# Kernel tuning notes

Measured on AMD Instinct MI355X. Metric: run time of the kernel, lower is better.

The kernel has to match this reference:

```python
import jax, jax.numpy as jnp
import numpy as np

# Module config (matches init_kwargs)
G, K, S = 64, 3, 2          # base patch size, num scales, scale factor
B, H, W, C = 64, 512, 512, 3
HG, HL = 128, 128
D_IN = K * G * G * C


def setup_inputs() -> dict:
    key = jax.random.key(0)
    kx, kl, k1, k2 = jax.random.split(key, 4)
    x = jax.random.normal(kx, (B, H, W, C), dtype=jnp.float32)
    # glimpse locations in [-1, 1)
    l = jax.random.uniform(kl, (B, 2), minval=-1.0, maxval=1.0, dtype=jnp.float32)
    # fc1: phi (D_IN -> HG); fc2: l (2 -> HL). PyTorch-Linear-like scale.
    W1 = jax.random.normal(k1, (D_IN, HG), dtype=jnp.float32) / np.sqrt(D_IN)
    b1 = jnp.zeros((HG,), dtype=jnp.float32)
    W2 = jax.random.normal(k2, (2, HL), dtype=jnp.float32) / np.sqrt(2.0)
    b2 = jnp.zeros((HL,), dtype=jnp.float32)
    return {"x": x, "l": l, "W1": W1, "b1": b1, "W2": W2, "b2": b2}


def _extract_glimpse(x, l):
    """Retina: k multi-scale patches centered at l, resized to (G,G).
    Returns (B, K, G, G, C)."""
    sizes = [G * S**i for i in range(K)]              # 64, 128, 256
    pad = sizes[-1] // 2 + 1                          # pad once for largest scale
    xp = jnp.pad(x, ((0, 0), (pad, pad), (pad, pad), (0, 0)))
    # denormalize: [-1,1] -> [0,H], truncated to int (torch .long())
    coords = (0.5 * (l + 1.0) * H).astype(jnp.int32)  # (B,2): col0=x, col1=y
    patches = []
    for size in sizes:
        fy = coords[:, 1] - size // 2 + pad
        fx = coords[:, 0] - size // 2 + pad

        def slice_one(img, y0, x0, size=size):
            return jax.lax.dynamic_slice(img, (y0, x0, 0), (size, size, C))

        p = jax.vmap(slice_one)(xp, fy, fx)           # (B, size, size, C)
        f = size // G
        if f > 1:  # downsample by integer factor via average pooling
            p = p.reshape(B, G, f, G, f, C).mean(axis=(2, 4))
        patches.append(p)
    return jnp.stack(patches, axis=1)                 # (B, K, G, G, C)


def reference(x, l, W1, b1, W2, b2):
    phi = _extract_glimpse(x, l).reshape(x.shape[0], -1)   # (B, K*G*G*C)
    phi_out = jax.nn.relu(phi @ W1 + b1)                   # (B, HG)
    l_out = jax.nn.relu(l @ W2 + b2)                       # (B, HL)
    return jax.nn.relu(jnp.concatenate([phi_out, l_out], axis=1))
```

## Files before the change

kernel.cpp:

```cpp
#include <hip/hip_runtime.h>
#include <hip/hip_bf16.h>

#define G_     64
#define NK     3
#define NB     64
#define IH     512
#define IW     512
#define NC     3
#define HG_    128
#define HL_    128
#define D_IN_    (NK * G_ * G_ * NC)
#define D_SCALE  (G_ * G_ * NC)
#define KCH      128
#define NCHUNK   (D_IN_ / KCH)
#define BSPLIT   4
#define NBLK     (NCHUNK * BSPLIT)
#define PSTRIDE  (NB * HG_)

template <int F>
__device__ __forceinline__ void scale_body(
    const float* __restrict__ x, const float* __restrict__ l,
    const float* __restrict__ W1, float* __restrict__ P,
    int roff, int d0, int b0, int chunkGlobal,
    float (&phi_s)[16][KCH], int* cx_s, int* cy_s)
{
    const int tid = threadIdx.x;
    if (tid < 16) {
        float lx = l[(b0 + tid) * 2 + 0];
        float ly = l[(b0 + tid) * 2 + 1];
        cx_s[tid] = (int)((0.5f * (lx + 1.0f)) * 512.0f);
        cy_s[tid] = (int)((0.5f * (ly + 1.0f)) * 512.0f);
    }
    __syncthreads();

    const int dd   = tid & (KCH - 1);
    const int jb0  = (tid >> 7) * 8;
    const int r    = roff + dd;
    const int gy   = r / (G_ * NC);
    const int rem  = r - gy * (G_ * NC);
    const int gx   = rem / NC;
    const int c    = rem - gx * NC;
    constexpr float inv = 1.0f / (float)(F * F);
    constexpr int JU = (F == 4) ? 2 : 8;

#pragma unroll 1
    for (int jo = 0; jo < 8; jo += JU) {
        float sums[JU];
#pragma unroll
        for (int ji = 0; ji < JU; ++ji) {
            const int jb = jb0 + jo + ji;
            const int b  = b0 + jb;
            const int by = cy_s[jb] - 32 * F + gy * F;
            const int bx = cx_s[jb] - 32 * F + gx * F;
            const float* bimg = x + (size_t)b * (IH * IW * NC) + c;
            float s = 0.0f;
#pragma unroll
            for (int dy = 0; dy < F; ++dy) {
                const int y = by + dy;
                const bool yok = (unsigned)y < (unsigned)IH;
#pragma unroll
                for (int dx = 0; dx < F; ++dx) {
                    const int xx = bx + dx;
                    const bool ok = yok && ((unsigned)xx < (unsigned)IW);
                    s += ok ? bimg[(size_t)y * (IW * NC) + xx * NC] : 0.0f;
                }
            }
            sums[ji] = s;
        }
#pragma unroll
        for (int ji = 0; ji < JU; ++ji)
            phi_s[jb0 + jo + ji][dd] = sums[ji] * inv;
    }
    __syncthreads();

    const int h0 = (tid & 31) * 4;
    const int bl = (tid >> 5) * 2;
    float a0[4] = {0, 0, 0, 0}, a1[4] = {0, 0, 0, 0};
    const float* wp = W1 + (size_t)d0 * HG_ + h0;
    const float4* prow0 = (const float4*)phi_s[bl];
    const float4* prow1 = (const float4*)phi_s[bl + 1];

#pragma unroll 2
    for (int t = 0; t < KCH / 4; ++t) {
        float4 p0v = prow0[t];
        float4 p1v = prow1[t];
#pragma unroll
        for (int u = 0; u < 4; ++u) {
            float4 wv = *(const float4*)(wp + (size_t)(4 * t + u) * HG_);
            float p0 = (&p0v.x)[u];
            float p1 = (&p1v.x)[u];
            a0[0] = fmaf(p0, wv.x, a0[0]);
            a0[1] = fmaf(p0, wv.y, a0[1]);
            a0[2] = fmaf(p0, wv.z, a0[2]);
            a0[3] = fmaf(p0, wv.w, a0[3]);
            a1[0] = fmaf(p1, wv.x, a1[0]);
            a1[1] = fmaf(p1, wv.y, a1[1]);
            a1[2] = fmaf(p1, wv.z, a1[2]);
            a1[3] = fmaf(p1, wv.w, a1[3]);
        }
    }
    float* pb = P + (size_t)chunkGlobal * PSTRIDE + (b0 + bl) * HG_ + h0;
    *(float4*)pb            = make_float4(a0[0], a0[1], a0[2], a0[3]);
    *(float4*)(pb + HG_)    = make_float4(a1[0], a1[1], a1[2], a1[3]);
}

__global__ __launch_bounds__(256) void fused(
    const float* __restrict__ x, const float* __restrict__ l,
    const float* __restrict__ W1, float* __restrict__ P)
{
    __shared__ float phi_s[16][KCH];
    __shared__ int cx_s[16], cy_s[16];

    const int chunkGlobal = blockIdx.x >> 2;
    const int b0 = (blockIdx.x & 3) * 16;
    const int d0 = chunkGlobal * KCH;
    const int chunkLocal = chunkGlobal % 96;
    const int roff = chunkLocal * KCH;

    if (chunkGlobal < 96) {
        scale_body<1>(x, l, W1, P, roff, d0, b0, chunkGlobal, phi_s, cx_s, cy_s);
    } else if (chunkGlobal < 192) {
        scale_body<2>(x, l, W1, P, roff, d0, b0, chunkGlobal, phi_s, cx_s, cy_s);
    } else {
        scale_body<4>(x, l, W1, P, roff, d0, b0, chunkGlobal, phi_s, cx_s, cy_s);
    }
}

__global__ __launch_bounds__(256) void reduce_epilogue(
    const float* __restrict__ P,
    const float* __restrict__ l,
    const float* __restrict__ b1,
    const float* __restrict__ W2,
    const float* __restrict__ b2,
    float* __restrict__ out)
{
    __shared__ float red[HG_];
    const int b = blockIdx.x;
    const int t = threadIdx.x;
    const int h = t & (HG_ - 1);
    const int half = t >> 7;

    float s = 0.0f;
    const float* p = P + (size_t)(half * 144) * PSTRIDE + b * HG_ + h;
#pragma unroll 8
    for (int c = 0; c < 144; ++c)
        s += p[(size_t)c * PSTRIDE];

    if (half == 1) red[h] = s;
    __syncthreads();

    if (half == 0) {
        out[b * (HG_ + HL_) + h] = fmaxf(s + red[h] + b1[h], 0.0f);
    } else {
        float l0 = l[b * 2 + 0];
        float l1 = l[b * 2 + 1];
        float v = fmaf(l1, W2[HL_ + h], fmaf(l0, W2[h], b2[h]));
        out[b * (HG_ + HL_) + HG_ + h] = fmaxf(v, 0.0f);
    }
}

extern "C" void kernel_launch(void* const* d_in, const int* in_sizes, int n_in,
                              void* d_out, int out_size, void* d_ws, size_t ws_size,
                              hipStream_t stream) {
    const float* x  = (const float*)d_in[0];
    const float* l  = (const float*)d_in[1];
    const float* W1 = (const float*)d_in[2];
    const float* b1 = (const float*)d_in[3];
    const float* W2 = (const float*)d_in[4];
    const float* b2 = (const float*)d_in[5];
    float* out = (float*)d_out;
    float* P = (float*)d_ws;

    fused<<<NBLK, 256, 0, stream>>>(x, l, W1, P);
    reduce_epilogue<<<NB, 256, 0, stream>>>(P, l, b1, W2, b2, out);
}
```

Before: 288.5 us.

## Split K across thread groups in GEMM tile and widen reduce kernel with float4

The per-block GEMM now gives each thread 4 batch rows instead of 2 and splits the 128-wide K chunk between two halves of the block. The two halves' partials are combined through shared memory before the store. Each W1 load is therefore reused across more rows, at the cost of an extra sync and more shared memory. The reduce epilogue moves to 512 threads, with 16 groups reading float4 partials over 18 chunks each and a final shared-memory reduction, to raise memory-level parallelism.

```diff
diff --git a/kernel.cpp b/kernel.cpp
--- a/kernel.cpp
+++ b/kernel.cpp
@@ -1,5 +1,4 @@
 #include <hip/hip_runtime.h>
-#include <hip/hip_bf16.h>
 
 #define G_     64
 #define NK     3
@@ -22,7 +21,7 @@
     const float* __restrict__ x, const float* __restrict__ l,
     const float* __restrict__ W1, float* __restrict__ P,
     int roff, int d0, int b0, int chunkGlobal,
-    float (&phi_s)[16][KCH], int* cx_s, int* cy_s)
+    float (&phi_s)[16][KCH], float (&red2)[16][HG_], int* cx_s, int* cy_s)
 {
     const int tid = threadIdx.x;
     if (tid < 16) {
@@ -73,35 +72,65 @@
     }
     __syncthreads();
 
-    const int h0 = (tid & 31) * 4;
-    const int bl = (tid >> 5) * 2;
-    float a0[4] = {0, 0, 0, 0}, a1[4] = {0, 0, 0, 0};
-    const float* wp = W1 + (size_t)d0 * HG_ + h0;
-    const float4* prow0 = (const float4*)phi_s[bl];
-    const float4* prow1 = (const float4*)phi_s[bl + 1];
+    const int hq  = tid & 31;
+    const int h0  = hq * 4;
+    const int gg  = tid >> 5;
+    const int bg4 = (gg & 3) * 4;
+    const int dh  = gg >> 2;
+    const int db  = dh * 64;
+
+    float4 a0 = {0.f, 0.f, 0.f, 0.f};
+    float4 a1 = {0.f, 0.f, 0.f, 0.f};
+    float4 a2 = {0.f, 0.f, 0.f, 0.f};
+    float4 a3 = {0.f, 0.f, 0.f, 0.f};
+    const float* wp = W1 + (size_t)(d0 + db) * HG_ + h0;
 
 #pragma unroll 2
-    for (int t = 0; t < KCH / 4; ++t) {
-        float4 p0v = prow0[t];
-        float4 p1v = prow1[t];
+    for (int t = 0; t < 16; ++t) {
+        const float4 pv0 = *(const float4*)&phi_s[bg4 + 0][db + 4 * t];
+        const float4 pv1 = *(const float4*)&phi_s[bg4 + 1][db + 4 * t];
+        const float4 pv2 = *(const float4*)&phi_s[bg4 + 2][db + 4 * t];
+        const float4 pv3 = *(const float4*)&phi_s[bg4 + 3][db + 4 * t];
 #pragma unroll
         for (int u = 0; u < 4; ++u) {
-            float4 wv = *(const float4*)(wp + (size_t)(4 * t + u) * HG_);
-            float p0 = (&p0v.x)[u];
-            float p1 = (&p1v.x)[u];
-            a0[0] = fmaf(p0, wv.x, a0[0]);
-            a0[1] = fmaf(p0, wv.y, a0[1]);
-            a0[2] = fmaf(p0, wv.z, a0[2]);
-            a0[3] = fmaf(p0, wv.w, a0[3]);
-            a1[0] = fmaf(p1, wv.x, a1[0]);
-            a1[1] = fmaf(p1, wv.y, a1[1]);
-            a1[2] = fmaf(p1, wv.z, a1[2]);
-            a1[3] = fmaf(p1, wv.w, a1[3]);
+            const float4 wv = *(const float4*)(wp + (size_t)(4 * t + u) * HG_);
+            const float p0 = (&pv0.x)[u];
+            const float p1 = (&pv1.x)[u];
+            const float p2 = (&pv2.x)[u];
+            const float p3 = (&pv3.x)[u];
+            a0.x = fmaf(p0, wv.x, a0.x); a0.y = fmaf(p0, wv.y, a0.y);
+            a0.z = fmaf(p0, wv.z, a0.z); a0.w = fmaf(p0, wv.w, a0.w);
+            a1.x = fmaf(p1, wv.x, a1.x); a1.y = fmaf(p1, wv.y, a1.y);
+            a1.z = fmaf(p1, wv.z, a1.z); a1.w = fmaf(p1, wv.w, a1.w);
+            a2.x = fmaf(p2, wv.x, a2.x); a2.y = fmaf(p2, wv.y, a2.y);
+            a2.z = fmaf(p2, wv.z, a2.z); a2.w = fmaf(p2, wv.w, a2.w);
+            a3.x = fmaf(p3, wv.x, a3.x); a3.y = fmaf(p3, wv.y, a3.y);
+            a3.z = fmaf(p3, wv.z, a3.z); a3.w = fmaf(p3, wv.w, a3.w);
         }
     }
-    float* pb = P + (size_t)chunkGlobal * PSTRIDE + (b0 + bl) * HG_ + h0;
-    *(float4*)pb            = make_float4(a0[0], a0[1], a0[2], a0[3]);
-    *(float4*)(pb + HG_)    = make_float4(a1[0], a1[1], a1[2], a1[3]);
+
+    if (dh == 1) {
+        *(float4*)&red2[bg4 + 0][h0] = a0;
+        *(float4*)&red2[bg4 + 1][h0] = a1;
+        *(float4*)&red2[bg4 + 2][h0] = a2;
+        *(float4*)&red2[bg4 + 3][h0] = a3;
+    }
+    __syncthreads();
+    if (dh == 0) {
+        float* pb = P + (size_t)chunkGlobal * PSTRIDE + (size_t)(b0 + bg4) * HG_ + h0;
+        const float4 r0 = *(const float4*)&red2[bg4 + 0][h0];
+        const float4 r1 = *(const float4*)&red2[bg4 + 1][h0];
+        const float4 r2 = *(const float4*)&red2[bg4 + 2][h0];
+        const float4 r3 = *(const float4*)&red2[bg4 + 3][h0];
+        *(float4*)(pb + 0 * HG_) =
+            make_float4(a0.x + r0.x, a0.y + r0.y, a0.z + r0.z, a0.w + r0.w);
+        *(float4*)(pb + 1 * HG_) =
+            make_float4(a1.x + r1.x, a1.y + r1.y, a1.z + r1.z, a1.w + r1.w);
+        *(float4*)(pb + 2 * HG_) =
+            make_float4(a2.x + r2.x, a2.y + r2.y, a2.z + r2.z, a2.w + r2.w);
+        *(float4*)(pb + 3 * HG_) =
+            make_float4(a3.x + r3.x, a3.y + r3.y, a3.z + r3.z, a3.w + r3.w);
+    }
 }
 
 __global__ __launch_bounds__(256) void fused(
@@ -109,6 +138,7 @@
     const float* __restrict__ W1, float* __restrict__ P)
 {
     __shared__ float phi_s[16][KCH];
+    __shared__ float red2[16][HG_];
     __shared__ int cx_s[16], cy_s[16];
 
     const int chunkGlobal = blockIdx.x >> 2;
@@ -118,15 +148,15 @@
     const int roff = chunkLocal * KCH;
 
     if (chunkGlobal < 96) {
-        scale_body<1>(x, l, W1, P, roff, d0, b0, chunkGlobal, phi_s, cx_s, cy_s);
+        scale_body<1>(x, l, W1, P, roff, d0, b0, chunkGlobal, phi_s, red2, cx_s, cy_s);
     } else if (chunkGlobal < 192) {
-        scale_body<2>(x, l, W1, P, roff, d0, b0, chunkGlobal, phi_s, cx_s, cy_s);
+        scale_body<2>(x, l, W1, P, roff, d0, b0, chunkGlobal, phi_s, red2, cx_s, cy_s);
     } else {
-        scale_body<4>(x, l, W1, P, roff, d0, b0, chunkGlobal, phi_s, cx_s, cy_s);
-    }
-}
-
-__global__ __launch_bounds__(256) void reduce_epilogue(
+        scale_body<4>(x, l, W1, P, roff, d0, b0, chunkGlobal, phi_s, red2, cx_s, cy_s);
+    }
+}
+
+__global__ __launch_bounds__(512) void reduce_epilogue(
     const float* __restrict__ P,
     const float* __restrict__ l,
     const float* __restrict__ b1,
@@ -134,28 +164,44 @@
     const float* __restrict__ b2,
     float* __restrict__ out)
 {
-    __shared__ float red[HG_];
-    const int b = blockIdx.x;
-    const int t = threadIdx.x;
-    const int h = t & (HG_ - 1);
-    const int half = t >> 7;
-
-    float s = 0.0f;
-    const float* p = P + (size_t)(half * 144) * PSTRIDE + b * HG_ + h;
-#pragma unroll 8
-    for (int c = 0; c < 144; ++c)
-        s += p[(size_t)c * PSTRIDE];
-
-    if (half == 1) red[h] = s;
-    __syncthreads();
-
-    if (half == 0) {
-        out[b * (HG_ + HL_) + h] = fmaxf(s + red[h] + b1[h], 0.0f);
-    } else {
-        float l0 = l[b * 2 + 0];
-        float l1 = l[b * 2 + 1];
-        float v = fmaf(l1, W2[HL_ + h], fmaf(l0, W2[h], b2[h]));
-        out[b * (HG_ + HL_) + HG_ + h] = fmaxf(v, 0.0f);
+    __shared__ float4 red[16][32];
+    const int b   = blockIdx.x;
+    const int t   = threadIdx.x;
+    const int hq  = t & 31;
+    const int grp = t >> 5;
+
+    const float4* p4 = (const float4*)P
+                     + (size_t)(grp * 18) * (PSTRIDE / 4)
+                     + (size_t)b * (HG_ / 4) + hq;
+    float sx = 0.f, sy = 0.f, sz = 0.f, sw = 0.f;
+#pragma unroll 9
+    for (int i = 0; i < 18; ++i) {
+        const float4 v = p4[(size_t)i * (PSTRIDE / 4)];
+        sx += v.x; sy += v.y; sz += v.z; sw += v.w;
+    }
+    red[grp][hq] = make_float4(sx, sy, sz, sw);
+    __syncthreads();
+
+    if (t < 32) {
+        float4 a = red[0][t];
+#pragma unroll
+        for (int g2 = 1; g2 < 16; ++g2) {
+            const float4 v = red[g2][t];
+            a.x += v.x; a.y += v.y; a.z += v.z; a.w += v.w;
+        }
+        const float4 bb = ((const float4*)b1)[t];
+        float4 o;
+        o.x = fmaxf(a.x + bb.x, 0.0f);
+        o.y = fmaxf(a.y + bb.y, 0.0f);
+        o.z = fmaxf(a.z + bb.z, 0.0f);
+        o.w = fmaxf(a.w + bb.w, 0.0f);
+        ((float4*)out)[(size_t)b * ((HG_ + HL_) / 4) + t] = o;
+    } else if (t >= 64 && t < 192) {
+        const int h = t - 64;
+        const float l0 = l[b * 2 + 0];
+        const float l1 = l[b * 2 + 1];
+        const float v = fmaf(l1, W2[HL_ + h], fmaf(l0, W2[h], b2[h]));
+        out[(size_t)b * (HG_ + HL_) + HG_ + h] = fmaxf(v, 0.0f);
     }
 }
 
@@ -172,5 +218,5 @@
     float* P = (float*)d_ws;
 
     fused<<<NBLK, 256, 0, stream>>>(x, l, W1, P);
-    reduce_epilogue<<<NB, 256, 0, stream>>>(P, l, b1, W2, b2, out);
-}
+    reduce_epilogue<<<NB, 512, 0, stream>>>(P, l, b1, W2, b2, out);
+}
```

Result: faster. 278.2 us (-3.6%).
